# Kernel tuning notes

Hardware: AMD Instinct MI355X
Metric: run time of the kernel (lower is better)

## Reference

```python
import jax, jax.numpy as jnp
import numpy as np

N, E, C, H, DE, B = 50000, 400000, 64, 4, 16, 64
EPS = 1e-5
NEG_SLOPE = 0.2
NBLOCKS = 2


def setup_inputs() -> dict:
    key = jax.random.key(0)
    ks = jax.random.split(key, 8)
    x = jax.random.normal(ks[0], (N, C), jnp.float32)
    edge_index = jax.random.randint(ks[1], (2, E), 0, N, dtype=jnp.int64)
    edge_attr = jax.random.normal(ks[2], (E, DE), jnp.float32)
    batch = jnp.sort(jax.random.randint(ks[3], (N,), 0, B, dtype=jnp.int64))
    s = 1.0 / np.sqrt(C)
    # stacked params for the 2 blocks
    Wl = jax.random.normal(ks[4], (NBLOCKS, C, H * C), jnp.float32) * s
    Wr = jax.random.normal(ks[5], (NBLOCKS, C, H * C), jnp.float32) * s
    We = jax.random.normal(ks[6], (NBLOCKS, DE, H * C), jnp.float32) * (1.0 / np.sqrt(DE))
    att = jax.random.normal(ks[7], (NBLOCKS, H, C), jnp.float32) * s
    gat_bias = jnp.zeros((NBLOCKS, C), jnp.float32)
    gn_weight = jnp.ones((NBLOCKS, C), jnp.float32)
    gn_bias = jnp.zeros((NBLOCKS, C), jnp.float32)
    gn_mean_scale = jnp.ones((NBLOCKS, C), jnp.float32)
    return dict(x=x, edge_index=edge_index, edge_attr=edge_attr, batch=batch,
                Wl=Wl, Wr=Wr, We=We, att=att, gat_bias=gat_bias,
                gn_weight=gn_weight, gn_bias=gn_bias, gn_mean_scale=gn_mean_scale)


def _segment_mean(v, seg, num):
    s = jax.ops.segment_sum(v, seg, num_segments=num)
    cnt = jax.ops.segment_sum(jnp.ones((v.shape[0], 1), v.dtype), seg, num_segments=num)
    return s / jnp.maximum(cnt, 1.0)


def _graph_norm(x, batch, w, b, ms):
    mean = _segment_mean(x, batch, B)                 # [B, C]
    sub = x - ms * mean[batch]
    var = _segment_mean(sub * sub, batch, B)          # [B, C]
    return sub / jnp.sqrt(var[batch] + EPS) * w + b


def _gatv2(x, src, dst, ea, Wl, Wr, We, att, bias):
    # src/dst/ea already include self loops (E2 = E + N edges)
    xl = (x @ Wl).reshape(N, H, C)                    # source transform
    xr = (x @ Wr).reshape(N, H, C)                    # target transform
    ee = (ea @ We).reshape(-1, H, C)                  # [E2, H, C]
    f = jax.nn.leaky_relu(xl[src] + xr[dst] + ee, NEG_SLOPE)
    logits = jnp.einsum('ehc,hc->eh', f, att)         # [E2, H]
    m = jax.ops.segment_max(logits, dst, num_segments=N)
    a = jnp.exp(logits - m[dst])
    denom = jax.ops.segment_sum(a, dst, num_segments=N)
    alpha = a / denom[dst]                            # per-target softmax
    out = jax.ops.segment_sum(xl[src] * alpha[:, :, None], dst, num_segments=N)
    return out.mean(axis=1) + bias                    # concat=False -> head mean


def reference(x, edge_index, edge_attr, batch, Wl, Wr, We, att, gat_bias,
              gn_weight, gn_bias, gn_mean_scale):
    loop = jnp.arange(N, dtype=edge_index.dtype)
    src = jnp.concatenate([edge_index[0], loop])
    dst = jnp.concatenate([edge_index[1], loop])
    # add_self_loops with fill_value='mean'
    ea = jnp.concatenate([edge_attr,
                          jnp.broadcast_to(edge_attr.mean(axis=0), (N, DE))])
    residual = x
    for i in range(NBLOCKS):
        h = _graph_norm(x, batch, gn_weight[i], gn_bias[i], gn_mean_scale[i])
        h = jax.nn.relu(h)
        x = _gatv2(h, src, dst, ea, Wl[i], Wr[i], We[i], att[i], gat_bias[i])
    return x + residual
```

## Files before the change

### kernel.cpp

```cpp
#include <hip/hip_runtime.h>
#include <math.h>

#define NN 50000
#define EE 400000
#define ETOT 450000
#define CC 64
#define HH 4
#define DEA 16
#define NBATCH 64
#define HC 256
#define EPSV 1e-5f
#define NB 49
#define NGB 782
#define NPW 2

typedef unsigned short ushort_t;
typedef unsigned int uint_t;
using h2t = decltype(__builtin_amdgcn_cvt_pkrtz(0.0f, 0.0f));

__device__ __forceinline__ float4 ld4(const float* p){ return *(const float4*)p; }
__device__ __forceinline__ int rfl(int v){ return __builtin_amdgcn_readfirstlane(v); }
__device__ __forceinline__ ushort_t f2b(float f){
  uint_t u = __float_as_uint(f);
  uint_t r = (u + 0x7FFFu + ((u >> 16) & 1u)) >> 16;
  return (ushort_t)r;
}
__device__ __forceinline__ float b2f_lo(uint_t u){ return __uint_as_float(u << 16); }
__device__ __forceinline__ float b2f_hi(uint_t u){ return __uint_as_float(u & 0xFFFF0000u); }
__device__ __forceinline__ uint_t h2u(h2t h){ return __builtin_bit_cast(uint_t, h); }
__device__ __forceinline__ h2t u2h(uint_t u){ return __builtin_bit_cast(h2t, u); }

template<int CTRL>
__device__ __forceinline__ float dpp_add(float x){
  int y = __builtin_amdgcn_update_dpp(0, __float_as_int(x), CTRL, 0xF, 0xF, true);
  return x + __int_as_float(y);
}
__device__ __forceinline__ float red16(float x){
  x = dpp_add<0xB1>(x);
  x = dpp_add<0x4E>(x);
  x = dpp_add<0x141>(x);
  x = dpp_add<0x140>(x);
  return x;
}

__global__ void k_easum(const float* __restrict__ ea, float* __restrict__ easum){
  int tid = threadIdx.x;
  int gid = blockIdx.x*256 + tid;
  int gsz = gridDim.x*256;
  float s = 0.f;
  for (long long i = gid; i < (long long)EE*DEA; i += gsz) s += ea[i];
  __shared__ float sd[256];
  sd[tid] = s; __syncthreads();
  if (tid < DEA){
    float t = 0.f;
    for (int j = tid; j < 256; j += DEA) t += sd[j];
    atomicAdd(&easum[tid], t);
  }
}

__global__ void k_hist(const int* __restrict__ dst, int* __restrict__ cnt){
  int e = blockIdx.x*256 + threadIdx.x;
  if (e < ETOT){
    int d = (e < EE) ? dst[e] : (e - EE);
    atomicAdd(&cnt[d], 1);
  }
}

__global__ __launch_bounds__(1024)
void k_scan1(const int* __restrict__ cnt, int* __restrict__ loc, int* __restrict__ bsum){
  __shared__ int wsum[16];
  int tid = threadIdx.x, lane = tid & 63, wv = tid >> 6;
  int i = blockIdx.x*1024 + tid;
  int v = (i < NN) ? cnt[i] : 0;
  int incl = v;
  #pragma unroll
  for (int off = 1; off < 64; off <<= 1){
    int t = __shfl_up(incl, off, 64);
    if (lane >= off) incl += t;
  }
  if (lane == 63) wsum[wv] = incl;
  __syncthreads();
  if (wv == 0){
    int s = (lane < 16) ? wsum[lane] : 0;
    #pragma unroll
    for (int off = 1; off < 16; off <<= 1){
      int t = __shfl_up(s, off, 64);
      if (lane >= off) s += t;
    }
    if (lane < 16) wsum[lane] = s;
  }
  __syncthreads();
  int excl = (wv ? wsum[wv-1] : 0) + incl - v;
  if (i < NN) loc[i] = excl;
  if (tid == 1023) bsum[blockIdx.x] = wsum[15];
}

__global__ void k_scan2(int* __restrict__ bsum, int* __restrict__ row_ptr){
  int lane = threadIdx.x;
  int v = (lane < NB) ? bsum[lane] : 0;
  int incl = v;
  #pragma unroll
  for (int off = 1; off < 64; off <<= 1){
    int t = __shfl_up(incl, off, 64);
    if (lane >= off) incl += t;
  }
  if (lane < NB) bsum[lane] = incl - v;
  if (lane == 63) row_ptr[NN] = incl;
}

__global__ __launch_bounds__(1024)
void k_scan3(const int* __restrict__ loc, const int* __restrict__ bsum,
             int* __restrict__ row_ptr, int* __restrict__ wp){
  int i = blockIdx.x*1024 + threadIdx.x;
  if (i < NN){
    int v = loc[i] + bsum[blockIdx.x];
    row_ptr[i] = v; wp[i] = v;
  }
}

__global__ void k_scatter(const int* __restrict__ dst, const int* __restrict__ src,
                          const float* __restrict__ ea, const float* __restrict__ easum,
                          int* __restrict__ wp, int* __restrict__ csrc,
                          uint_t* __restrict__ eas){
  int e = blockIdx.x*256 + threadIdx.x;
  if (e >= ETOT) return;
  int d, s;
  if (e < EE){ d = dst[e]; s = src[e]; } else { d = e - EE; s = d; }
  int pos = atomicAdd(&wp[d], 1);
  csrc[pos] = s;
  float buf[16];
  if (e < EE){
    #pragma unroll
    for (int q = 0; q < 4; q++){
      float4 v = ld4(ea + (size_t)e*DEA + q*4);
      buf[q*4+0]=v.x; buf[q*4+1]=v.y; buf[q*4+2]=v.z; buf[q*4+3]=v.w;
    }
  } else {
    const float invE = 1.0f / (float)EE;
    #pragma unroll
    for (int k = 0; k < 16; k++) buf[k] = easum[k]*invE;
  }
  uint_t pk[8];
  #pragma unroll
  for (int p = 0; p < 8; p++)
    pk[p] = h2u(__builtin_amdgcn_cvt_pkrtz(buf[2*p], buf[2*p+1]));
  *(uint4*)(eas + (size_t)pos*8 + 0) = make_uint4(pk[0], pk[1], pk[2], pk[3]);
  *(uint4*)(eas + (size_t)pos*8 + 4) = make_uint4(pk[4], pk[5], pk[6], pk[7]);
}

__global__ void k_packw(const float* __restrict__ Wl, const float* __restrict__ Wr,
                        ushort_t* __restrict__ Wp){
  int t = blockIdx.x*256 + threadIdx.x;
  if (t >= 16384) return;
  int c4 = (t & 63) * 4;
  int k = (t >> 6) & 63;
  int mat = (t >> 12) & 1;
  int l = t >> 13;
  const float* W = (mat ? Wr : Wl) + (size_t)l*CC*HC;
  float4 w = ld4(W + (size_t)k*HC + c4);
  uint2 o;
  o.x = (uint_t)f2b(w.x) | ((uint_t)f2b(w.y) << 16);
  o.y = (uint_t)f2b(w.z) | ((uint_t)f2b(w.w) << 16);
  *(uint2*)(Wp + ((size_t)((l*2+mat)*64 + k))*HC + c4) = o;
}

__global__ __launch_bounds__(256)
void k_stats(const float* __restrict__ x, const int* __restrict__ batch,
             float* __restrict__ S, float* __restrict__ Q){
  int c = threadIdx.x & 63, g = threadIdx.x >> 6;
  int r0 = blockIdx.x*256;
  int hiR = r0 + 256; if (hiR > NN) hiR = NN;
  float s = 0.f, q = 0.f;
  int curb = -1;
  for (int n = r0 + g; n < hiR; n += 4){
    int b = batch[n];
    if (b != curb){
      if (curb >= 0){ atomicAdd(&S[curb*64+c], s); atomicAdd(&Q[curb*64+c], q); }
      curb = b; s = 0.f; q = 0.f;
    }
    float v = x[(size_t)n*CC + c];
    s += v; q += v*v;
  }
  if (curb >= 0){ atomicAdd(&S[curb*64+c], s); atomicAdd(&Q[curb*64+c], q); }
}

__device__ __forceinline__ int lowerb(const int* a, int n, int key){
  int lo = 0, hi = n;
  while (lo < hi){ int mid = (lo+hi) >> 1; if (a[mid] < key) lo = mid+1; else hi = mid; }
  return lo;
}

__global__ void k_fin(const float* __restrict__ S, const float* __restrict__ Q,
                      const int* __restrict__ batch,
                      const float* __restrict__ w, const float* __restrict__ bb,
                      const float* __restrict__ ms,
                      float* __restrict__ scale, float* __restrict__ shift){
  __shared__ float cntf;
  int b = blockIdx.x, c = threadIdx.x;
  if (c == 0){
    int lo = lowerb(batch, NN, b), hi = lowerb(batch, NN, b+1);
    cntf = fmaxf((float)(hi - lo), 1.f);
  }
  __syncthreads();
  float inv = 1.f / cntf;
  float m = S[b*64+c] * inv;
  float a = ms[c] * m;
  float var = Q[b*64+c]*inv - 2.f*a*m + a*a;
  var = fmaxf(var, 0.f);
  float rstd = rsqrtf(var + EPSV);
  float sc = rstd * w[c];
  scale[b*64+c] = sc;
  shift[b*64+c] = bb[c] - a*sc;
}

__global__ __launch_bounds__(256)
void k_gemm(const float* __restrict__ x, const int* __restrict__ batch,
            const float* __restrict__ scale, const float* __restrict__ shift,
            const ushort_t* __restrict__ WpA, const ushort_t* __restrict__ WpB,
            ushort_t* __restrict__ outA, ushort_t* __restrict__ outB){
  const ushort_t* Wp = blockIdx.z ? WpB : WpA;
  ushort_t* out = blockIdx.z ? outB : outA;
  int n0 = blockIdx.x * 64;
  __shared__ float hT[64][72];
  int tid = threadIdx.x;
  for (int t = tid; t < 1024; t += 256){
    int r = t >> 4, ch = t & 15;
    int n = n0 + r;
    float4 v = make_float4(0.f,0.f,0.f,0.f);
    if (n < NN){
      int b = batch[n];
      v = ld4(x + (size_t)n*CC + ch*4);
      float4 sc = ld4(scale + b*64 + ch*4);
      float4 sh = ld4(shift + b*64 + ch*4);
      v.x = fmaxf(v.x*sc.x + sh.x, 0.f);
      v.y = fmaxf(v.y*sc.y + sh.y, 0.f);
      v.z = fmaxf(v.z*sc.z + sh.z, 0.f);
      v.w = fmaxf(v.w*sc.w + sh.w, 0.f);
    }
    hT[ch*4+0][r] = v.x; hT[ch*4+1][r] = v.y; hT[ch*4+2][r] = v.z; hT[ch*4+3][r] = v.w;
  }
  __syncthreads();
  int c = tid & 63, rg = tid >> 6;
  int r0 = rg * 16;
  float acc[16][4];
  #pragma unroll
  for (int i = 0; i < 16; i++){ acc[i][0]=0.f; acc[i][1]=0.f; acc[i][2]=0.f; acc[i][3]=0.f; }
  #pragma unroll 4
  for (int k = 0; k < 64; k++){
    float4 a0 = *(const float4*)&hT[k][r0+0];
    float4 a1 = *(const float4*)&hT[k][r0+4];
    float4 a2 = *(const float4*)&hT[k][r0+8];
    float4 a3 = *(const float4*)&hT[k][r0+12];
    uint2 wv = *(const uint2*)(Wp + (size_t)k*HC + c*4);
    float b0 = b2f_lo(wv.x), b1 = b2f_hi(wv.x), b2 = b2f_lo(wv.y), b3 = b2f_hi(wv.y);
    const float av[16] = {a0.x,a0.y,a0.z,a0.w, a1.x,a1.y,a1.z,a1.w,
                          a2.x,a2.y,a2.z,a2.w, a3.x,a3.y,a3.z,a3.w};
    #pragma unroll
    for (int i = 0; i < 16; i++){
      acc[i][0] += av[i]*b0; acc[i][1] += av[i]*b1;
      acc[i][2] += av[i]*b2; acc[i][3] += av[i]*b3;
    }
  }
  #pragma unroll
  for (int i = 0; i < 16; i++){
    int n = n0 + r0 + i;
    if (n < NN){
      uint2 o;
      o.x = (uint_t)f2b(acc[i][0]) | ((uint_t)f2b(acc[i][1]) << 16);
      o.y = (uint_t)f2b(acc[i][2]) | ((uint_t)f2b(acc[i][3]) << 16);
      *(uint2*)(out + (size_t)n*HC + c*4) = o;
    }
  }
}

__global__ __launch_bounds__(256, 4)
void k_gat(const int* __restrict__ row_ptr, const int* __restrict__ csrc,
           const uint_t* __restrict__ eas,
           const ushort_t* __restrict__ xlh, const ushort_t* __restrict__ xrh,
           const float* __restrict__ We, const float* __restrict__ att,
           const float* __restrict__ bias, const float* __restrict__ resid,
           float* __restrict__ out){
  int lane = threadIdx.x & 63;
  int h = lane >> 4, cg = lane & 15;
  int col = h*64 + cg*4;
  int wid = (blockIdx.x*256 + threadIdx.x) >> 6;
  int n0 = wid * NPW;
  if (n0 >= NN) return;
  int n1 = n0 + NPW; if (n1 > NN) n1 = NN;

  uint_t werh[4][8];
  #pragma unroll
  for (int p = 0; p < 8; p++){
    float4 w0 = ld4(We + (size_t)(2*p+0)*HC + col);
    float4 w1 = ld4(We + (size_t)(2*p+1)*HC + col);
    werh[0][p] = h2u(__builtin_amdgcn_cvt_pkrtz(w0.x, w1.x));
    werh[1][p] = h2u(__builtin_amdgcn_cvt_pkrtz(w0.y, w1.y));
    werh[2][p] = h2u(__builtin_amdgcn_cvt_pkrtz(w0.z, w1.z));
    werh[3][p] = h2u(__builtin_amdgcn_cvt_pkrtz(w0.w, w1.w));
  }
  #pragma unroll
  for (int j = 0; j < 4; j++)
    #pragma unroll
    for (int p = 0; p < 8; p++)
      asm volatile("" : "+v"(werh[j][p]));

  float4 attv = ld4(att + col);
  float4 biasv = ld4(bias + cg*4);

  for (int n = n0; n < n1; n++){
    int rr0 = rfl(row_ptr[n]), rr1 = rfl(row_ptr[n+1]);
    uint2 xrp = *(const uint2*)(xrh + (size_t)n*HC + col);
    float xr0 = b2f_lo(xrp.x), xr1 = b2f_hi(xrp.x);
    float xr2 = b2f_lo(xrp.y), xr3 = b2f_hi(xrp.y);
    float m = -3.4e38f, dsum = 0.f;
    float a0 = 0.f, a1 = 0.f, a2 = 0.f, a3 = 0.f;

    int sC = rfl(csrc[rr0]);
    uint2 xlp = *(const uint2*)(xlh + (size_t)sC*HC + col);
    uint_t earC[8];
    {
      const uint_t* ep = eas + (size_t)rr0*8;
      #pragma unroll
      for (int p = 0; p < 8; p++) earC[p] = ep[p];
    }

    for (int idx = rr0; idx < rr1; idx++){
      int idn = (idx+1 < rr1) ? idx+1 : rr0;
      int sN = rfl(csrc[idn]);
      uint2 xlq = *(const uint2*)(xlh + (size_t)sN*HC + col);
      uint_t earN[8];
      {
        const uint_t* ep = eas + (size_t)rfl(idn)*8;
        #pragma unroll
        for (int p = 0; p < 8; p++) earN[p] = ep[p];
      }

      float xl0 = b2f_lo(xlp.x), xl1 = b2f_hi(xlp.x);
      float xl2 = b2f_lo(xlp.y), xl3 = b2f_hi(xlp.y);

      float p0 = 0.f, p1 = 0.f, p2 = 0.f, p3 = 0.f;
      #pragma unroll
      for (int p = 0; p < 8; p++){
        h2t e = u2h(earC[p]);
        p0 = __builtin_amdgcn_fdot2(e, u2h(werh[0][p]), p0, false);
        p1 = __builtin_amdgcn_fdot2(e, u2h(werh[1][p]), p1, false);
        p2 = __builtin_amdgcn_fdot2(e, u2h(werh[2][p]), p2, false);
        p3 = __builtin_amdgcn_fdot2(e, u2h(werh[3][p]), p3, false);
      }
      float v0 = xl0 + xr0 + p0; v0 = (v0 > 0.f) ? v0 : 0.2f*v0;
      float v1 = xl1 + xr1 + p1; v1 = (v1 > 0.f) ? v1 : 0.2f*v1;
      float v2 = xl2 + xr2 + p2; v2 = (v2 > 0.f) ? v2 : 0.2f*v2;
      float v3 = xl3 + xr3 + p3; v3 = (v3 > 0.f) ? v3 : 0.2f*v3;
      float pl = v0*attv.x + v1*attv.y + v2*attv.z + v3*attv.w;
      pl = red16(pl);

      float mn = fmaxf(m, pl);
      float sc = __expf(m - mn);
      float wexp = __expf(pl - mn);
      dsum = dsum*sc + wexp;
      a0 = a0*sc + wexp*xl0;
      a1 = a1*sc + wexp*xl1;
      a2 = a2*sc + wexp*xl2;
      a3 = a3*sc + wexp*xl3;
      m = mn;

      xlp = xlq;
      #pragma unroll
      for (int p = 0; p < 8; p++) earC[p] = earN[p];
    }

    float inv = 1.0f / dsum;
    float o0 = a0*inv, o1 = a1*inv, o2 = a2*inv, o3 = a3*inv;
    #pragma unroll
    for (int off = 16; off < 64; off <<= 1){
      o0 += __shfl_xor(o0, off, 64);
      o1 += __shfl_xor(o1, off, 64);
      o2 += __shfl_xor(o2, off, 64);
      o3 += __shfl_xor(o3, off, 64);
    }
    if (lane < 16){
      float r0v = o0*0.25f + biasv.x;
      float r1v = o1*0.25f + biasv.y;
      float r2v = o2*0.25f + biasv.z;
      float r3v = o3*0.25f + biasv.w;
      if (resid){
        float4 rv = ld4(resid + (size_t)n*CC + cg*4);
        r0v += rv.x; r1v += rv.y; r2v += rv.z; r3v += rv.w;
      }
      *(float4*)(out + (size_t)n*CC + cg*4) = make_float4(r0v, r1v, r2v, r3v);
    }
  }
}

extern "C" void kernel_launch(void* const* d_in, const int* in_sizes, int n_in,
                              void* d_out, int out_size, void* d_ws, size_t ws_size,
                              hipStream_t stream) {
  const float* x     = (const float*)d_in[0];
  const int*   ei    = (const int*)d_in[1];
  const int*   src   = ei;
  const int*   dst   = ei + EE;
  const float* ea    = (const float*)d_in[2];
  const int*   batch = (const int*)d_in[3];
  const float* Wl    = (const float*)d_in[4];
  const float* Wr    = (const float*)d_in[5];
  const float* We    = (const float*)d_in[6];
  const float* att   = (const float*)d_in[7];
  const float* gb    = (const float*)d_in[8];
  const float* gw    = (const float*)d_in[9];
  const float* gnb   = (const float*)d_in[10];
  const float* gms   = (const float*)d_in[11];
  float* out = (float*)d_out;

  char* ws = (char*)d_ws;
  size_t off = 0;
  auto alloc = [&](size_t bytes) -> void* {
    void* p = ws + off; off += (bytes + 255) & ~(size_t)255; return p;
  };
  int*   cnt     = (int*)alloc(NN*sizeof(int));
  int*   loc     = (int*)alloc(NN*sizeof(int));
  int*   bsum    = (int*)alloc(64*sizeof(int));
  int*   wp      = (int*)alloc(NN*sizeof(int));
  int*   row_ptr = (int*)alloc((NN+1)*sizeof(int));
  int*   csrc    = (int*)alloc((size_t)ETOT*sizeof(int));
  uint_t* eas    = (uint_t*)alloc((size_t)ETOT*8*sizeof(uint_t));
  float* easum   = (float*)alloc(64);
  float* statSQ  = (float*)alloc(4*4096*sizeof(float));
  float* scaleb  = (float*)alloc(4096*sizeof(float));
  float* shiftb  = (float*)alloc(4096*sizeof(float));
  ushort_t* Wp   = (ushort_t*)alloc((size_t)4*64*HC*sizeof(ushort_t));
  ushort_t* xlh  = (ushort_t*)alloc((size_t)NN*HC*sizeof(ushort_t));
  ushort_t* xrh  = (ushort_t*)alloc((size_t)NN*HC*sizeof(ushort_t));
  float* xbuf    = (float*)alloc((size_t)NN*CC*sizeof(float));
  if (off > ws_size) return;

  hipMemsetAsync(cnt, 0, NN*sizeof(int), stream);
  hipMemsetAsync(easum, 0, 64, stream);
  hipMemsetAsync(statSQ, 0, 4*4096*sizeof(float), stream);
  k_easum<<<1024, 256, 0, stream>>>(ea, easum);
  k_hist<<<(ETOT+255)/256, 256, 0, stream>>>(dst, cnt);
  k_scan1<<<NB, 1024, 0, stream>>>(cnt, loc, bsum);
  k_scan2<<<1, 64, 0, stream>>>(bsum, row_ptr);
  k_scan3<<<NB, 1024, 0, stream>>>(loc, bsum, row_ptr, wp);
  k_scatter<<<(ETOT+255)/256, 256, 0, stream>>>(dst, src, ea, easum, wp, csrc, eas);
  k_packw<<<64, 256, 0, stream>>>(Wl, Wr, Wp);

  int gatBlocks = (NN + NPW*4 - 1) / (NPW*4);
  for (int i = 0; i < 2; i++){
    const float* xin = i ? xbuf : x;
    float* S = statSQ + i*4096;
    float* Q = statSQ + 2*4096 + i*4096;
    k_stats<<<(NN+255)/256, 256, 0, stream>>>(xin, batch, S, Q);
    k_fin<<<64, 64, 0, stream>>>(S, Q, batch, gw + i*CC, gnb + i*CC, gms + i*CC, scaleb, shiftb);
    k_gemm<<<dim3(NGB, 1, 2), 256, 0, stream>>>(xin, batch, scaleb, shiftb,
                                                Wp + (size_t)(i*2+0)*64*HC,
                                                Wp + (size_t)(i*2+1)*64*HC,
                                                xlh, xrh);
    k_gat<<<gatBlocks, 256, 0, stream>>>(row_ptr, csrc, eas, xlh, xrh,
                                         We + (size_t)i*DEA*HC, att + i*HH*CC,
                                         gb + i*CC, i ? x : nullptr, i ? out : xbuf);
  }
}
```

Measured before the change: 410.9 us.

## Use fp16 dot2 in node GEMM and fuse preprocessing kernels and memsets

```diff
diff --git a/kernel.cpp b/kernel.cpp
--- a/kernel.cpp
+++ b/kernel.cpp
@@ -13,6 +13,8 @@
 #define NB 49
 #define NGB 782
 #define NPW 2
+#define HISTB 1758
+#define PACKB 128
 
 typedef unsigned short ushort_t;
 typedef unsigned int uint_t;
@@ -43,26 +45,28 @@
   return x;
 }
 
-__global__ void k_easum(const float* __restrict__ ea, float* __restrict__ easum){
+__global__ __launch_bounds__(256)
+void k_pre1(const float* __restrict__ ea, const int* __restrict__ dst,
+            float* __restrict__ easum, int* __restrict__ cnt){
   int tid = threadIdx.x;
-  int gid = blockIdx.x*256 + tid;
-  int gsz = gridDim.x*256;
-  float s = 0.f;
-  for (long long i = gid; i < (long long)EE*DEA; i += gsz) s += ea[i];
-  __shared__ float sd[256];
-  sd[tid] = s; __syncthreads();
-  if (tid < DEA){
-    float t = 0.f;
-    for (int j = tid; j < 256; j += DEA) t += sd[j];
-    atomicAdd(&easum[tid], t);
-  }
-}
-
-__global__ void k_hist(const int* __restrict__ dst, int* __restrict__ cnt){
-  int e = blockIdx.x*256 + threadIdx.x;
+  int bid = blockIdx.x;
+  int e = bid*256 + tid;
   if (e < ETOT){
     int d = (e < EE) ? dst[e] : (e - EE);
     atomicAdd(&cnt[d], 1);
+  }
+  if (bid < 1024){
+    int gid = bid*256 + tid;
+    const int gsz = 262144;
+    float s = 0.f;
+    for (long long i = gid; i < (long long)EE*DEA; i += gsz) s += ea[i];
+    __shared__ float sd[256];
+    sd[tid] = s; __syncthreads();
+    if (tid < DEA){
+      float t = 0.f;
+      for (int j = tid; j < 256; j += DEA) t += sd[j];
+      atomicAdd(&easum[tid], t);
+    }
   }
 }
 
@@ -118,50 +122,50 @@
   }
 }
 
-__global__ void k_scatter(const int* __restrict__ dst, const int* __restrict__ src,
-                          const float* __restrict__ ea, const float* __restrict__ easum,
-                          int* __restrict__ wp, int* __restrict__ csrc,
-                          uint_t* __restrict__ eas){
-  int e = blockIdx.x*256 + threadIdx.x;
-  if (e >= ETOT) return;
-  int d, s;
-  if (e < EE){ d = dst[e]; s = src[e]; } else { d = e - EE; s = d; }
-  int pos = atomicAdd(&wp[d], 1);
-  csrc[pos] = s;
-  float buf[16];
-  if (e < EE){
+__global__ __launch_bounds__(256)
+void k_pre2(const int* __restrict__ dst, const int* __restrict__ src,
+            const float* __restrict__ ea, const float* __restrict__ easum,
+            int* __restrict__ wp, int* __restrict__ csrc, uint_t* __restrict__ eas,
+            const float* __restrict__ Wl, const float* __restrict__ Wr,
+            uint_t* __restrict__ Wq){
+  int bid = blockIdx.x;
+  int tid = threadIdx.x;
+  if (bid < HISTB){
+    int e = bid*256 + tid;
+    if (e >= ETOT) return;
+    int d, s;
+    if (e < EE){ d = dst[e]; s = src[e]; } else { d = e - EE; s = d; }
+    int pos = atomicAdd(&wp[d], 1);
+    csrc[pos] = s;
+    float buf[16];
+    if (e < EE){
+      #pragma unroll
+      for (int q = 0; q < 4; q++){
+        float4 v = ld4(ea + (size_t)e*DEA + q*4);
+        buf[q*4+0]=v.x; buf[q*4+1]=v.y; buf[q*4+2]=v.z; buf[q*4+3]=v.w;
+      }
+    } else {
+      const float invE = 1.0f / (float)EE;
+      #pragma unroll
+      for (int k = 0; k < 16; k++) buf[k] = easum[k]*invE;
+    }
+    uint_t pk[8];
     #pragma unroll
-    for (int q = 0; q < 4; q++){
-      float4 v = ld4(ea + (size_t)e*DEA + q*4);
-      buf[q*4+0]=v.x; buf[q*4+1]=v.y; buf[q*4+2]=v.z; buf[q*4+3]=v.w;
-    }
+    for (int p = 0; p < 8; p++)
+      pk[p] = h2u(__builtin_amdgcn_cvt_pkrtz(buf[2*p], buf[2*p+1]));
+    *(uint4*)(eas + (size_t)pos*8 + 0) = make_uint4(pk[0], pk[1], pk[2], pk[3]);
+    *(uint4*)(eas + (size_t)pos*8 + 4) = make_uint4(pk[4], pk[5], pk[6], pk[7]);
   } else {
-    const float invE = 1.0f / (float)EE;
-    #pragma unroll
-    for (int k = 0; k < 16; k++) buf[k] = easum[k]*invE;
-  }
-  uint_t pk[8];
-  #pragma unroll
-  for (int p = 0; p < 8; p++)
-    pk[p] = h2u(__builtin_amdgcn_cvt_pkrtz(buf[2*p], buf[2*p+1]));
-  *(uint4*)(eas + (size_t)pos*8 + 0) = make_uint4(pk[0], pk[1], pk[2], pk[3]);
-  *(uint4*)(eas + (size_t)pos*8 + 4) = make_uint4(pk[4], pk[5], pk[6], pk[7]);
-}
-
-__global__ void k_packw(const float* __restrict__ Wl, const float* __restrict__ Wr,
-                        ushort_t* __restrict__ Wp){
-  int t = blockIdx.x*256 + threadIdx.x;
-  if (t >= 16384) return;
-  int c4 = (t & 63) * 4;
-  int k = (t >> 6) & 63;
-  int mat = (t >> 12) & 1;
-  int l = t >> 13;
-  const float* W = (mat ? Wr : Wl) + (size_t)l*CC*HC;
-  float4 w = ld4(W + (size_t)k*HC + c4);
-  uint2 o;
-  o.x = (uint_t)f2b(w.x) | ((uint_t)f2b(w.y) << 16);
-  o.y = (uint_t)f2b(w.z) | ((uint_t)f2b(w.w) << 16);
-  *(uint2*)(Wp + ((size_t)((l*2+mat)*64 + k))*HC + c4) = o;
+    int t = (bid - HISTB)*256 + tid;
+    int col = t & 255;
+    int kp  = (t >> 8) & 31;
+    int lm  = t >> 13;
+    int l = lm >> 1, mat = lm & 1;
+    const float* W = (mat ? Wr : Wl) + (size_t)l*CC*HC;
+    float w0 = W[(size_t)(2*kp+0)*HC + col];
+    float w1 = W[(size_t)(2*kp+1)*HC + col];
+    Wq[(size_t)lm*8192 + kp*256 + col] = h2u(__builtin_amdgcn_cvt_pkrtz(w0, w1));
+  }
 }
 
 __global__ __launch_bounds__(256)
@@ -216,12 +220,12 @@
 __global__ __launch_bounds__(256)
 void k_gemm(const float* __restrict__ x, const int* __restrict__ batch,
             const float* __restrict__ scale, const float* __restrict__ shift,
-            const ushort_t* __restrict__ WpA, const ushort_t* __restrict__ WpB,
+            const uint_t* __restrict__ WqA, const uint_t* __restrict__ WqB,
             ushort_t* __restrict__ outA, ushort_t* __restrict__ outB){
-  const ushort_t* Wp = blockIdx.z ? WpB : WpA;
+  const uint_t* Wq = blockIdx.z ? WqB : WqA;
   ushort_t* out = blockIdx.z ? outB : outA;
   int n0 = blockIdx.x * 64;
-  __shared__ float hT[64][72];
+  __shared__ uint_t hTp[32][72];
   int tid = threadIdx.x;
   for (int t = tid; t < 1024; t += 256){
     int r = t >> 4, ch = t & 15;
@@ -237,7 +241,8 @@
       v.z = fmaxf(v.z*sc.z + sh.z, 0.f);
       v.w = fmaxf(v.w*sc.w + sh.w, 0.f);
     }
-    hT[ch*4+0][r] = v.x; hT[ch*4+1][r] = v.y; hT[ch*4+2][r] = v.z; hT[ch*4+3][r] = v.w;
+    hTp[ch*2+0][r] = h2u(__builtin_amdgcn_cvt_pkrtz(v.x, v.y));
+    hTp[ch*2+1][r] = h2u(__builtin_amdgcn_cvt_pkrtz(v.z, v.w));
   }
   __syncthreads();
   int c = tid & 63, rg = tid >> 6;
@@ -246,19 +251,22 @@
   #pragma unroll
   for (int i = 0; i < 16; i++){ acc[i][0]=0.f; acc[i][1]=0.f; acc[i][2]=0.f; acc[i][3]=0.f; }
   #pragma unroll 4
-  for (int k = 0; k < 64; k++){
-    float4 a0 = *(const float4*)&hT[k][r0+0];
-    float4 a1 = *(const float4*)&hT[k][r0+4];
-    float4 a2 = *(const float4*)&hT[k][r0+8];
-    float4 a3 = *(const float4*)&hT[k][r0+12];
-    uint2 wv = *(const uint2*)(Wp + (size_t)k*HC + c*4);
-    float b0 = b2f_lo(wv.x), b1 = b2f_hi(wv.x), b2 = b2f_lo(wv.y), b3 = b2f_hi(wv.y);
-    const float av[16] = {a0.x,a0.y,a0.z,a0.w, a1.x,a1.y,a1.z,a1.w,
-                          a2.x,a2.y,a2.z,a2.w, a3.x,a3.y,a3.z,a3.w};
+  for (int kp = 0; kp < 32; kp++){
+    uint4 a0 = *(const uint4*)&hTp[kp][r0+0];
+    uint4 a1 = *(const uint4*)&hTp[kp][r0+4];
+    uint4 a2 = *(const uint4*)&hTp[kp][r0+8];
+    uint4 a3 = *(const uint4*)&hTp[kp][r0+12];
+    uint4 wv = *(const uint4*)(Wq + (size_t)kp*256 + c*4);
+    h2t w0 = u2h(wv.x), w1 = u2h(wv.y), w2 = u2h(wv.z), w3 = u2h(wv.w);
+    const uint_t av[16] = {a0.x,a0.y,a0.z,a0.w, a1.x,a1.y,a1.z,a1.w,
+                           a2.x,a2.y,a2.z,a2.w, a3.x,a3.y,a3.z,a3.w};
     #pragma unroll
     for (int i = 0; i < 16; i++){
-      acc[i][0] += av[i]*b0; acc[i][1] += av[i]*b1;
-      acc[i][2] += av[i]*b2; acc[i][3] += av[i]*b3;
+      h2t e = u2h(av[i]);
+      acc[i][0] = __builtin_amdgcn_fdot2(e, w0, acc[i][0], false);
+      acc[i][1] = __builtin_amdgcn_fdot2(e, w1, acc[i][1], false);
+      acc[i][2] = __builtin_amdgcn_fdot2(e, w2, acc[i][2], false);
+      acc[i][3] = __builtin_amdgcn_fdot2(e, w3, acc[i][3], false);
     }
   }
   #pragma unroll
@@ -417,32 +425,29 @@
     void* p = ws + off; off += (bytes + 255) & ~(size_t)255; return p;
   };
   int*   cnt     = (int*)alloc(NN*sizeof(int));
+  float* easum   = (float*)alloc(64*sizeof(float));
+  float* statSQ  = (float*)alloc(4*4096*sizeof(float));
+  size_t zbytes  = off;
   int*   loc     = (int*)alloc(NN*sizeof(int));
   int*   bsum    = (int*)alloc(64*sizeof(int));
   int*   wp      = (int*)alloc(NN*sizeof(int));
   int*   row_ptr = (int*)alloc((NN+1)*sizeof(int));
   int*   csrc    = (int*)alloc((size_t)ETOT*sizeof(int));
   uint_t* eas    = (uint_t*)alloc((size_t)ETOT*8*sizeof(uint_t));
-  float* easum   = (float*)alloc(64);
-  float* statSQ  = (float*)alloc(4*4096*sizeof(float));
   float* scaleb  = (float*)alloc(4096*sizeof(float));
   float* shiftb  = (float*)alloc(4096*sizeof(float));
-  ushort_t* Wp   = (ushort_t*)alloc((size_t)4*64*HC*sizeof(ushort_t));
+  uint_t* Wq     = (uint_t*)alloc((size_t)4*8192*sizeof(uint_t));
   ushort_t* xlh  = (ushort_t*)alloc((size_t)NN*HC*sizeof(ushort_t));
   ushort_t* xrh  = (ushort_t*)alloc((size_t)NN*HC*sizeof(ushort_t));
   float* xbuf    = (float*)alloc((size_t)NN*CC*sizeof(float));
   if (off > ws_size) return;
 
-  hipMemsetAsync(cnt, 0, NN*sizeof(int), stream);
-  hipMemsetAsync(easum, 0, 64, stream);
-  hipMemsetAsync(statSQ, 0, 4*4096*sizeof(float), stream);
-  k_easum<<<1024, 256, 0, stream>>>(ea, easum);
-  k_hist<<<(ETOT+255)/256, 256, 0, stream>>>(dst, cnt);
+  hipMemsetAsync(cnt, 0, zbytes, stream);
+  k_pre1<<<HISTB, 256, 0, stream>>>(ea, dst, easum, cnt);
   k_scan1<<<NB, 1024, 0, stream>>>(cnt, loc, bsum);
   k_scan2<<<1, 64, 0, stream>>>(bsum, row_ptr);
   k_scan3<<<NB, 1024, 0, stream>>>(loc, bsum, row_ptr, wp);
-  k_scatter<<<(ETOT+255)/256, 256, 0, stream>>>(dst, src, ea, easum, wp, csrc, eas);
-  k_packw<<<64, 256, 0, stream>>>(Wl, Wr, Wp);
+  k_pre2<<<HISTB + PACKB, 256, 0, stream>>>(dst, src, ea, easum, wp, csrc, eas, Wl, Wr, Wq);
 
   int gatBlocks = (NN + NPW*4 - 1) / (NPW*4);
   for (int i = 0; i < 2; i++){
@@ -452,8 +457,8 @@
     k_stats<<<(NN+255)/256, 256, 0, stream>>>(xin, batch, S, Q);
     k_fin<<<64, 64, 0, stream>>>(S, Q, batch, gw + i*CC, gnb + i*CC, gms + i*CC, scaleb, shiftb);
     k_gemm<<<dim3(NGB, 1, 2), 256, 0, stream>>>(xin, batch, scaleb, shiftb,
-                                                Wp + (size_t)(i*2+0)*64*HC,
-                                                Wp + (size_t)(i*2+1)*64*HC,
+                                                Wq + (size_t)(i*2+0)*8192,
+                                                Wq + (size_t)(i*2+1)*8192,
                                                 xlh, xrh);
     k_gat<<<gatBlocks, 256, 0, stream>>>(row_ptr, csrc, eas, xlh, xrh,
                                          We + (size_t)i*DEA*HC, att + i*HH*CC,
```

New measurement: 382.6 us. 6.9% less time.
